# Performance work log

Measured on AMD Instinct MI355X. Metric: run time of the kernel, lower is better.

Reference implementation:

```python
import jax, jax.numpy as jnp
import numpy as np

N_NODES = 50000
N_EDGES = 800000
FEAT_DIM = 64
NUM_RELS = 8


def setup_inputs() -> dict:
    key = jax.random.key(0)
    k1, k2, k3, k4, k5 = jax.random.split(key, 5)
    features = jax.random.normal(k1, (N_NODES, FEAT_DIM), dtype=jnp.float32)
    # xavier_uniform with relu gain ~= sqrt(2)*sqrt(6/(D+D))
    limit = np.sqrt(2.0) * np.sqrt(6.0 / (FEAT_DIM + FEAT_DIM))
    weight_r = jax.random.uniform(k2, (NUM_RELS, FEAT_DIM, FEAT_DIM), dtype=jnp.float32,
                                  minval=-limit, maxval=limit)
    src = jax.random.randint(k3, (N_EDGES,), 0, N_NODES, dtype=jnp.int64 if jax.config.jax_enable_x64 else jnp.int32)
    dst = jax.random.randint(k4, (N_EDGES,), 0, N_NODES, dtype=src.dtype)
    etype = jax.random.randint(k5, (N_EDGES,), 0, NUM_RELS, dtype=src.dtype)
    return {"features": features, "weight_r": weight_r, "src": src, "dst": dst, "etype": etype}


def reference(features, weight_r, src, dst, etype):
    N, D = features.shape
    c = 0.2
    # in-degree of each destination node (DGL 'deg' node data)
    deg = jax.ops.segment_sum(jnp.ones(dst.shape, dtype=features.dtype), dst, num_segments=N)
    # relation-batched matmul: h @ W_r for every relation, then gather per edge.
    # [R, N, D] = 8*50000*64 floats -- cheap vs. materializing [E, D, D] weights.
    hw = jnp.einsum('nd,rdf->rnf', features, weight_r)
    msg = hw[etype, src] / deg[dst][:, None]          # [E, D]
    M = jax.ops.segment_sum(msg, dst, num_segments=N)  # scatter-sum mailbox reduce
    updated = jax.nn.relu(c * features + (1.0 - c) * M)
    # DGL only applies reduce to nodes that received messages; others keep h.
    return jnp.where((deg > 0)[:, None], updated, features)
```

## Files before the change

kernel.cpp:

```cpp
#include <hip/hip_runtime.h>
#include <hip/hip_bf16.h>

#define N_NODES 50000
#define N_EDGES 800000
#define FEAT 64
#define NRELS 8
#define NBUCK 196
#define EPB 2048
#define NBP 391
#define BCAP 5120

typedef __attribute__((ext_vector_type(8))) short bf16x8;
typedef __attribute__((ext_vector_type(4))) float f32x4;

static __host__ __device__ inline size_t align256(size_t x) { return (x + 255) & ~(size_t)255; }

__device__ inline unsigned short f2b(float f) {
    unsigned u = __builtin_bit_cast(unsigned, f);
    unsigned r = (u + 0x7fffu + ((u >> 16) & 1u)) >> 16;
    return (unsigned short)r;
}
__device__ inline float b2f(unsigned short u) {
    unsigned v = ((unsigned)u) << 16;
    return __builtin_bit_cast(float, v);
}

__global__ void bfill_kernel(const int* __restrict__ dst, const int* __restrict__ srcv,
                             const int* __restrict__ et, const float* __restrict__ W,
                             int* __restrict__ bcnt, int* __restrict__ tmp,
                             unsigned short* __restrict__ WtT, int E) {
    __shared__ int hist[256];
    __shared__ int base[256];
    __shared__ int lcur[256];
    const int t = threadIdx.x;
    hist[t] = 0; lcur[t] = 0;
    __syncthreads();
    const int e0 = blockIdx.x * EPB;
    int bk[8], pk[8];
#pragma unroll
    for (int k = 0; k < 8; k++) {
        int e = e0 + t + k * 256;
        if (e < E) {
            int dd = dst[e];
            bk[k] = dd >> 8;
            pk[k] = (srcv[e] & 0xFFFF) | (et[e] << 16) | ((dd & 255) << 19);
            atomicAdd(&hist[bk[k]], 1);
        } else bk[k] = -1;
    }
    __syncthreads();
    if (t < NBUCK && hist[t] > 0)
        base[t] = t * BCAP + atomicAdd(&bcnt[t], hist[t]);
    __syncthreads();
#pragma unroll
    for (int k = 0; k < 8; k++) {
        if (bk[k] >= 0) {
            int r = atomicAdd(&lcur[bk[k]], 1);
            int pos = base[bk[k]] + r;
            if (pos < (bk[k] + 1) * BCAP)
                tmp[pos] = pk[k];
        }
    }

    if (blockIdx.x < 32) {
        int i4 = blockIdx.x * 256 + t;
        float4 v = ((const float4*)W)[i4];
        int bse = i4 * 4;
        int f0 = bse & 63;
        int rd = bse >> 6;
        int d  = rd & 63;
        int r  = rd >> 6;
        unsigned short* w0 = WtT + ((size_t)(r * 64 + f0) * 64 + d);
        w0[0 * 64] = f2b(v.x);
        w0[1 * 64] = f2b(v.y);
        w0[2 * 64] = f2b(v.z);
        w0[3 * 64] = f2b(v.w);
    }
}

__global__ void sort3_kernel(const int* __restrict__ bcnt, const int* __restrict__ tmp,
                             int* __restrict__ spk, int* __restrict__ off_s,
                             int* __restrict__ off_e, int N) {
    __shared__ int s[256];
    __shared__ int cur[256];
    const int b = blockIdx.x;
    const int t = threadIdx.x;
    const int n0 = b * 256;
    const int nn = min(256, N - n0);
    const int s0 = b * BCAP;
    const int s1 = s0 + min(bcnt[b], BCAP);

    s[t] = 0;
    __syncthreads();
    for (int i = s0 + t; i < s1; i += 256)
        atomicAdd(&s[(tmp[i] >> 19) & 255], 1);
    __syncthreads();
    const int myc = s[t];
    for (int o = 1; o < 256; o <<= 1) {
        int u = (t >= o) ? s[t - o] : 0;
        __syncthreads();
        s[t] += u;
        __syncthreads();
    }
    const int ex = s0 + s[t] - myc;
    if (t < nn) {
        off_s[n0 + t] = ex;
        off_e[n0 + t] = ex + myc;
        cur[t] = ex;
    }
    __syncthreads();
    for (int i = s0 + t; i < s1; i += 256) {
        int e = tmp[i];
        int pos = atomicAdd(&cur[(e >> 19) & 255], 1);
        spk[pos] = e;
    }
}

__global__ void hwb_kernel(const float* __restrict__ feat,
                           const unsigned short* __restrict__ WtT,
                           unsigned short* __restrict__ hwb, int N) {
    __shared__ unsigned short Fl[64 * 72];
    __shared__ unsigned short Wt[2][64 * 72];
    __shared__ unsigned short Dl[2][64 * 72];
    const int n0 = blockIdx.x * 64;
    const int t  = threadIdx.x;

    const float4* F4 = (const float4*)feat;
#pragma unroll
    for (int i = 0; i < 4; i++) {
        int idx = t + 256 * i;
        int n = idx >> 4;
        int c = idx & 15;
        int gn = n0 + n;
        float4 v = make_float4(0.f, 0.f, 0.f, 0.f);
        if (gn < N) v = F4[(size_t)gn * 16 + c];
        ushort4 b;
        b.x = f2b(v.x); b.y = f2b(v.y); b.z = f2b(v.z); b.w = f2b(v.w);
        *(ushort4*)&Fl[n * 72 + c * 4] = b;
    }
    {
        const bf16x8* wsrc = (const bf16x8*)WtT;
#pragma unroll
        for (int j = 0; j < 2; j++) {
            int idx = t + 256 * j;
            int f = idx >> 3, d0 = (idx & 7) * 8;
            *(bf16x8*)&Wt[0][f * 72 + d0] = wsrc[idx];
        }
    }
    __syncthreads();

    const int w    = t >> 6;
    const int l    = t & 63;
    const int col  = l & 15;
    const int quad = l >> 4;

    const int arow = (w * 16 + col) * 72 + quad * 8;
    bf16x8 a0 = *(const bf16x8*)&Fl[arow];
    bf16x8 a1 = *(const bf16x8*)&Fl[arow + 32];

    for (int r = 0; r < NRELS; r++) {
        bf16x8 w0, w1;
        if (r + 1 < NRELS) {
            const bf16x8* wsrc = (const bf16x8*)(WtT + (size_t)(r + 1) * 4096);
            w0 = wsrc[t];
            w1 = wsrc[t + 256];
        }

        const unsigned short* wbuf = Wt[r & 1];
        unsigned short* dbuf = Dl[r & 1];
#pragma unroll
        for (int ft = 0; ft < 4; ft++) {
            const int brow = (ft * 16 + col) * 72 + quad * 8;
            bf16x8 b0 = *(const bf16x8*)&wbuf[brow];
            bf16x8 b1 = *(const bf16x8*)&wbuf[brow + 32];
            f32x4 acc = {0.f, 0.f, 0.f, 0.f};
            acc = __builtin_amdgcn_mfma_f32_16x16x32_bf16(a0, b0, acc, 0, 0, 0);
            acc = __builtin_amdgcn_mfma_f32_16x16x32_bf16(a1, b1, acc, 0, 0, 0);
#pragma unroll
            for (int i = 0; i < 4; i++)
                dbuf[(w * 16 + quad * 4 + i) * 72 + ft * 16 + col] = f2b(acc[i]);
        }
        if (r + 1 < NRELS) {
            int f0 = t >> 3, d0 = (t & 7) * 8;
            *(bf16x8*)&Wt[(r + 1) & 1][f0 * 72 + d0] = w0;
            int idx = t + 256;
            int f1 = idx >> 3, d1 = (idx & 7) * 8;
            *(bf16x8*)&Wt[(r + 1) & 1][f1 * 72 + d1] = w1;
        }
        __syncthreads();

        unsigned short* dstp = hwb + ((size_t)r * N + n0) * 64;
#pragma unroll
        for (int j0 = 0; j0 < 2; j0++) {
            int j = t + 256 * j0;
            int row = j >> 3, c = j & 7;
            if (n0 + row < N) {
                bf16x8 dv = *(const bf16x8*)&dbuf[row * 72 + c * 8];
                *(bf16x8*)(dstp + row * 64 + c * 8) = dv;
            }
        }
    }
}

__global__ void reduce_kernel(const int* __restrict__ off_s, const int* __restrict__ off_e,
                              const int* __restrict__ spk,
                              const unsigned short* __restrict__ hwb,
                              const float* __restrict__ feat,
                              float* __restrict__ out, int N) {
    const int node = blockIdx.x * 4 + (threadIdx.x >> 6);
    if (node >= N) return;
    const int lane = threadIdx.x & 63;
    const int g = lane >> 3, q = lane & 7;

    const int b = off_s[node], e = off_e[node];
    const int deg = e - b;

    float acc[8] = {0.f, 0.f, 0.f, 0.f, 0.f, 0.f, 0.f, 0.f};
    for (int i = b + g; i < e; i += 8) {
        int pk = spk[i];
        int s = pk & 0xFFFF, r = (pk >> 16) & 7;
        bf16x8 u = *(const bf16x8*)(hwb + ((size_t)r * N + s) * 64 + q * 8);
#pragma unroll
        for (int k = 0; k < 8; k++) acc[k] += b2f((unsigned short)u[k]);
    }
#pragma unroll
    for (int k = 0; k < 8; k++) {
        acc[k] += __shfl_xor(acc[k], 8);
        acc[k] += __shfl_xor(acc[k], 16);
        acc[k] += __shfl_xor(acc[k], 32);
    }

    if (g == 0) {
        const float4* fp = (const float4*)feat + (size_t)node * 16 + q * 2;
        float4 f0 = fp[0], f1 = fp[1];
        float4 r0, r1;
        if (deg > 0) {
            float inv = 0.8f / (float)deg;
            r0.x = fmaxf(0.2f * f0.x + acc[0] * inv, 0.f);
            r0.y = fmaxf(0.2f * f0.y + acc[1] * inv, 0.f);
            r0.z = fmaxf(0.2f * f0.z + acc[2] * inv, 0.f);
            r0.w = fmaxf(0.2f * f0.w + acc[3] * inv, 0.f);
            r1.x = fmaxf(0.2f * f1.x + acc[4] * inv, 0.f);
            r1.y = fmaxf(0.2f * f1.y + acc[5] * inv, 0.f);
            r1.z = fmaxf(0.2f * f1.z + acc[6] * inv, 0.f);
            r1.w = fmaxf(0.2f * f1.w + acc[7] * inv, 0.f);
        } else {
            r0 = f0; r1 = f1;
        }
        float4* op = (float4*)out + (size_t)node * 16 + q * 2;
        op[0] = r0;
        op[1] = r1;
    }
}

__global__ void degf_kernel(const int* __restrict__ dst, float* __restrict__ deg, int E) {
    int e = blockIdx.x * blockDim.x + threadIdx.x;
    if (e < E) atomicAdd(deg + dst[e], 1.0f);
}

__global__ void otf_kernel(const int* __restrict__ src, const int* __restrict__ dst,
                           const int* __restrict__ et, const float* __restrict__ feat,
                           const float* __restrict__ W, float* __restrict__ out, int E) {
    int wid = (blockIdx.x * blockDim.x + threadIdx.x) >> 6;
    int l = threadIdx.x & 63;
    if (wid >= E) return;
    int s = src[wid], dd = dst[wid], r = et[wid];
    float fv = feat[(size_t)s * 64 + l];
    const float* Wr = W + (size_t)r * 4096;
    float acc = 0.f;
#pragma unroll
    for (int d = 0; d < 64; d++) {
        float a = __shfl(fv, d);
        acc += a * Wr[d * 64 + l];
    }
    atomicAdd(out + (size_t)dd * 64 + l, acc);
}

__global__ void final_kernel(const float* __restrict__ feat, const float* __restrict__ deg,
                             float* __restrict__ out, int N) {
    int i = blockIdx.x * blockDim.x + threadIdx.x;
    if (i >= N * 16) return;
    int n = i >> 4;
    float d = deg[n];
    float4 f = ((const float4*)feat)[i];
    float4 m = ((float4*)out)[i];
    float4 res;
    if (d > 0.f) {
        float inv = 0.8f / d;
        res.x = fmaxf(0.2f * f.x + m.x * inv, 0.f);
        res.y = fmaxf(0.2f * f.y + m.y * inv, 0.f);
        res.z = fmaxf(0.2f * f.z + m.z * inv, 0.f);
        res.w = fmaxf(0.2f * f.w + m.w * inv, 0.f);
    } else {
        res = f;
    }
    ((float4*)out)[i] = res;
}

extern "C" void kernel_launch(void* const* d_in, const int* in_sizes, int n_in,
                              void* d_out, int out_size, void* d_ws, size_t ws_size,
                              hipStream_t stream) {
    const float* feat = (const float*)d_in[0];
    const float* W    = (const float*)d_in[1];
    const int*   src  = (const int*)d_in[2];
    const int*   dst  = (const int*)d_in[3];
    const int*   et   = (const int*)d_in[4];
    float* out = (float*)d_out;

    const int N = N_NODES, E = N_EDGES;

    char* p = (char*)d_ws;
    int* bcnt  = (int*)p;  p += align256((size_t)NBUCK * 4);
    int* off_s = (int*)p;  p += align256((size_t)N * 4);
    int* off_e = (int*)p;  p += align256((size_t)N * 4);
    int* tmp   = (int*)p;  p += align256((size_t)NBUCK * BCAP * 4);
    int* spk   = (int*)p;  p += align256((size_t)NBUCK * BCAP * 4);
    unsigned short* WtT = (unsigned short*)p;
    p += align256((size_t)NRELS * FEAT * FEAT * 2);
    unsigned short* hwb = (unsigned short*)p;
    p += (size_t)NRELS * N * FEAT * 2;
    size_t need_full = (size_t)(p - (char*)d_ws);

    if (ws_size >= need_full) {
        hipMemsetAsync(bcnt, 0, (size_t)NBUCK * 4, stream);
        bfill_kernel<<<NBP, 256, 0, stream>>>(dst, src, et, W, bcnt, tmp, WtT, E);
        sort3_kernel<<<NBUCK, 256, 0, stream>>>(bcnt, tmp, spk, off_s, off_e, N);
        hwb_kernel<<<(N + 63) / 64, 256, 0, stream>>>(feat, WtT, hwb, N);
        reduce_kernel<<<(N + 3) / 4, 256, 0, stream>>>(off_s, off_e, spk, hwb, feat, out, N);
    } else {
        float* deg = (float*)d_ws;
        hipMemsetAsync(out, 0, (size_t)N * FEAT * 4, stream);
        hipMemsetAsync(deg, 0, (size_t)N * 4, stream);
        degf_kernel<<<(E + 255) / 256, 256, 0, stream>>>(dst, deg, E);
        otf_kernel<<<(E + 3) / 4, 256, 0, stream>>>(src, dst, et, feat, W, out, E);
        final_kernel<<<(N * 16 + 255) / 256, 256, 0, stream>>>(feat, deg, out, N);
    }
}
```

Measured before the change: 143.4 us.

## Merge bucket sort and hw matmul into one launch; unroll reduce gather by two

The per-bucket counting sort and the bf16 feature-times-weight kernel run as one grid, with block ranges split by blockIdx, so the two independent stages overlap and one launch is removed. The reduce loop now processes two edges per iteration, issuing two independent hwb gathers so more memory requests are in flight. The merged kernel carries the shared memory of both stages, which may lower occupancy for the sort blocks.

New measurement: 131.5 us. 8.3% less time.

```diff
diff --git a/kernel.cpp b/kernel.cpp
--- a/kernel.cpp
+++ b/kernel.cpp
@@ -9,6 +9,7 @@
 #define EPB 2048
 #define NBP 391
 #define BCAP 5120
+#define HWB_BLOCKS 782
 
 typedef __attribute__((ext_vector_type(8))) short bf16x8;
 typedef __attribute__((ext_vector_type(4))) float f32x4;
@@ -77,52 +78,54 @@
     }
 }
 
-__global__ void sort3_kernel(const int* __restrict__ bcnt, const int* __restrict__ tmp,
-                             int* __restrict__ spk, int* __restrict__ off_s,
-                             int* __restrict__ off_e, int N) {
-    __shared__ int s[256];
-    __shared__ int cur[256];
-    const int b = blockIdx.x;
-    const int t = threadIdx.x;
-    const int n0 = b * 256;
-    const int nn = min(256, N - n0);
-    const int s0 = b * BCAP;
-    const int s1 = s0 + min(bcnt[b], BCAP);
-
-    s[t] = 0;
-    __syncthreads();
-    for (int i = s0 + t; i < s1; i += 256)
-        atomicAdd(&s[(tmp[i] >> 19) & 255], 1);
-    __syncthreads();
-    const int myc = s[t];
-    for (int o = 1; o < 256; o <<= 1) {
-        int u = (t >= o) ? s[t - o] : 0;
-        __syncthreads();
-        s[t] += u;
-        __syncthreads();
-    }
-    const int ex = s0 + s[t] - myc;
-    if (t < nn) {
-        off_s[n0 + t] = ex;
-        off_e[n0 + t] = ex + myc;
-        cur[t] = ex;
-    }
-    __syncthreads();
-    for (int i = s0 + t; i < s1; i += 256) {
-        int e = tmp[i];
-        int pos = atomicAdd(&cur[(e >> 19) & 255], 1);
-        spk[pos] = e;
-    }
-}
-
-__global__ void hwb_kernel(const float* __restrict__ feat,
+__global__ void mid_kernel(const int* __restrict__ bcnt, const int* __restrict__ tmp,
+                           int* __restrict__ spk, int* __restrict__ off_s,
+                           int* __restrict__ off_e,
+                           const float* __restrict__ feat,
                            const unsigned short* __restrict__ WtT,
                            unsigned short* __restrict__ hwb, int N) {
     __shared__ unsigned short Fl[64 * 72];
     __shared__ unsigned short Wt[2][64 * 72];
     __shared__ unsigned short Dl[2][64 * 72];
-    const int n0 = blockIdx.x * 64;
-    const int t  = threadIdx.x;
+    __shared__ int s[256];
+    __shared__ int cur[256];
+    const int t = threadIdx.x;
+
+    if (blockIdx.x < NBUCK) {
+        const int b = blockIdx.x;
+        const int n0 = b * 256;
+        const int nn = min(256, N - n0);
+        const int s0 = b * BCAP;
+        const int s1 = s0 + min(bcnt[b], BCAP);
+
+        s[t] = 0;
+        __syncthreads();
+        for (int i = s0 + t; i < s1; i += 256)
+            atomicAdd(&s[(tmp[i] >> 19) & 255], 1);
+        __syncthreads();
+        const int myc = s[t];
+        for (int o = 1; o < 256; o <<= 1) {
+            int u = (t >= o) ? s[t - o] : 0;
+            __syncthreads();
+            s[t] += u;
+            __syncthreads();
+        }
+        const int ex = s0 + s[t] - myc;
+        if (t < nn) {
+            off_s[n0 + t] = ex;
+            off_e[n0 + t] = ex + myc;
+            cur[t] = ex;
+        }
+        __syncthreads();
+        for (int i = s0 + t; i < s1; i += 256) {
+            int e = tmp[i];
+            int pos = atomicAdd(&cur[(e >> 19) & 255], 1);
+            spk[pos] = e;
+        }
+        return;
+    }
+
+    const int n0 = (blockIdx.x - NBUCK) * 64;
 
     const float4* F4 = (const float4*)feat;
 #pragma unroll
@@ -215,12 +218,22 @@
     const int deg = e - b;
 
     float acc[8] = {0.f, 0.f, 0.f, 0.f, 0.f, 0.f, 0.f, 0.f};
-    for (int i = b + g; i < e; i += 8) {
-        int pk = spk[i];
-        int s = pk & 0xFFFF, r = (pk >> 16) & 7;
-        bf16x8 u = *(const bf16x8*)(hwb + ((size_t)r * N + s) * 64 + q * 8);
-#pragma unroll
-        for (int k = 0; k < 8; k++) acc[k] += b2f((unsigned short)u[k]);
+    for (int i = b + g; i < e; i += 16) {
+        int pk0 = spk[i];
+        int i1 = i + 8;
+        int pk1 = (i1 < e) ? spk[i1] : -1;
+        int s0 = pk0 & 0xFFFF, r0 = (pk0 >> 16) & 7;
+        bf16x8 u0 = *(const bf16x8*)(hwb + ((size_t)r0 * N + s0) * 64 + q * 8);
+        if (pk1 >= 0) {
+            int s1 = pk1 & 0xFFFF, r1 = (pk1 >> 16) & 7;
+            bf16x8 u1 = *(const bf16x8*)(hwb + ((size_t)r1 * N + s1) * 64 + q * 8);
+#pragma unroll
+            for (int k = 0; k < 8; k++)
+                acc[k] += b2f((unsigned short)u0[k]) + b2f((unsigned short)u1[k]);
+        } else {
+#pragma unroll
+            for (int k = 0; k < 8; k++) acc[k] += b2f((unsigned short)u0[k]);
+        }
     }
 #pragma unroll
     for (int k = 0; k < 8; k++) {
@@ -323,8 +336,8 @@
     if (ws_size >= need_full) {
         hipMemsetAsync(bcnt, 0, (size_t)NBUCK * 4, stream);
         bfill_kernel<<<NBP, 256, 0, stream>>>(dst, src, et, W, bcnt, tmp, WtT, E);
-        sort3_kernel<<<NBUCK, 256, 0, stream>>>(bcnt, tmp, spk, off_s, off_e, N);
-        hwb_kernel<<<(N + 63) / 64, 256, 0, stream>>>(feat, WtT, hwb, N);
+        mid_kernel<<<NBUCK + HWB_BLOCKS, 256, 0, stream>>>(bcnt, tmp, spk, off_s, off_e,
+                                                           feat, WtT, hwb, N);
         reduce_kernel<<<(N + 3) / 4, 256, 0, stream>>>(off_s, off_e, spk, hwb, feat, out, N);
     } else {
         float* deg = (float*)d_ws;
```
